# Kernel optimization log

Measured on AMD Instinct MI355X. Metric: run time of the kernel, lower is better.

## Reference

```python
import jax, jax.numpy as jnp
import numpy as np

H = 10  # hidden_size


def _lstm_cell(x, h, c, Wih, Whh, bih, bhh):
    # PyTorch LSTMCell: gates ordered i, f, g, o
    gates = x @ Wih.T + bih + h @ Whh.T + bhh  # [B, 4H]
    i, f, g, o = jnp.split(gates, 4, axis=-1)
    c_new = jax.nn.sigmoid(f) * c + jax.nn.sigmoid(i) * jnp.tanh(g)
    h_new = jax.nn.sigmoid(o) * jnp.tanh(c_new)
    return h_new, c_new


def setup_inputs() -> dict:
    key = jax.random.key(0)
    ks = jax.random.split(key, 12)
    B, T = 16384, 2048
    s = 1.0 / np.sqrt(H)  # PyTorch LSTMCell init scale
    inp = {
        "x": jax.random.normal(ks[0], (B, T, 2), dtype=jnp.float32),
        "WihA": jax.random.uniform(ks[1], (4 * H, 2), minval=-s, maxval=s),
        "WhhA": jax.random.uniform(ks[2], (4 * H, H), minval=-s, maxval=s),
        "bihA": jax.random.uniform(ks[3], (4 * H,), minval=-s, maxval=s),
        "bhhA": jax.random.uniform(ks[4], (4 * H,), minval=-s, maxval=s),
        "WihB": jax.random.uniform(ks[5], (4 * H, 1), minval=-s, maxval=s),
        "WhhB": jax.random.uniform(ks[6], (4 * H, H), minval=-s, maxval=s),
        "bihB": jax.random.uniform(ks[7], (4 * H,), minval=-s, maxval=s),
        "bhhB": jax.random.uniform(ks[8], (4 * H,), minval=-s, maxval=s),
        "Wlin": jax.random.uniform(ks[9], (1, H), minval=-s, maxval=s),
        "blin": jax.random.uniform(ks[10], (1,), minval=-s, maxval=s),
    }
    return inp


def reference(x, WihA, WhhA, bihA, bhhA, WihB, WhhB, bihB, bhhB, Wlin, blin):
    B, T, _ = x.shape
    # time-major pairs: step 2k uses cellB on x[:, 2k, :1], step 2k+1 uses cellA on x[:, 2k+1, :]
    xs = jnp.transpose(x, (1, 0, 2)).reshape(T // 2, 2, B, 2)  # [T/2, 2, B, 2]
    h0 = jnp.zeros((B, H), dtype=x.dtype)
    c0 = jnp.zeros((B, H), dtype=x.dtype)

    def step(carry, x_pair):
        h, c = carry
        h, c = _lstm_cell(x_pair[0][:, :1], h, c, WihB, WhhB, bihB, bhhB)
        h, c = _lstm_cell(x_pair[1], h, c, WihA, WhhA, bihA, bhhA)
        return (h, c), None

    (h, c), _ = jax.lax.scan(step, (h0, c0), xs)
    # original stacks all hx but only uses the last timestep
    return jax.nn.sigmoid(h @ Wlin.T + blin)  # [B, 1]
```

## Files before the change

### kernel.cpp

```cpp
#include <hip/hip_runtime.h>
#include <math.h>

#define H 10
#define BATCH 16384
#define NPAIRS 1024
#define EPW 6

#define LOG2E 1.44269504088896340736f

#if __has_builtin(__builtin_amdgcn_exp2f)
#define EXP2(x) __builtin_amdgcn_exp2f(x)
#else
#define EXP2(x) exp2f(x)
#endif

__device__ __forceinline__ float fast_rcp(float x) { return __builtin_amdgcn_rcpf(x); }

__global__ void __launch_bounds__(64, 2)
lstm_kernel(const float* __restrict__ x,
            const float* __restrict__ WihA, const float* __restrict__ WhhA,
            const float* __restrict__ bihA, const float* __restrict__ bhhA,
            const float* __restrict__ WihB, const float* __restrict__ WhhB,
            const float* __restrict__ bihB, const float* __restrict__ bhhB,
            const float* __restrict__ Wlin, const float* __restrict__ blin,
            float* __restrict__ out)
{
    const int lane    = threadIdx.x;
    const int e_local = lane / H;
    const int j       = lane - e_local * H;
    const bool active = lane < EPW * H;
    const int elem    = blockIdx.x * EPW + e_local;
    const bool valid  = active && (elem < BATCH);
    const int jj      = active ? j : 0;
    const int elem_c  = valid ? elem : 0;

    float wA[4][H], wB[4][H];
    float bA[4], bB[4], wxA0[4], wxA1[4], wxB[4];
#pragma unroll
    for (int g = 0; g < 4; ++g) {
        const float s = (g == 2) ? (2.0f * LOG2E) : (-LOG2E);
        const int row = g * H + jj;
        bA[g]   = s * (bihA[row] + bhhA[row]);
        bB[g]   = s * (bihB[row] + bhhB[row]);
        wxA0[g] = s * WihA[row * 2 + 0];
        wxA1[g] = s * WihA[row * 2 + 1];
        wxB[g]  = s * WihB[row];
#pragma unroll
        for (int k = 0; k < H; ++k) {
            wA[g][k] = s * WhhA[row * H + k];
            wB[g][k] = s * WhhB[row * H + k];
        }
    }
#pragma unroll
    for (int g = 0; g < 4; ++g) {
        asm volatile("" : "+v"(bA[g]), "+v"(bB[g]), "+v"(wxA0[g]),
                          "+v"(wxA1[g]), "+v"(wxB[g]));
#pragma unroll
        for (int k = 0; k < H; ++k) {
            asm volatile("" : "+v"(wA[g][k]), "+v"(wB[g][k]));
        }
    }

    const int base4 = (e_local * H) << 2;
    const float4* __restrict__ xr = (const float4*)x + (size_t)elem_c * NPAIRS;

    float h = 0.0f, c = 0.0f;
    float4 xp = xr[0];

#pragma unroll 2
    for (int p = 0; p < NPAIRS; ++p) {
        const int pn = (p + 1 < NPAIRS) ? (p + 1) : p;
        const float4 xnext = xr[pn];

        {
            float y0 = fmaf(wxB[0], xp.x, bB[0]);
            float y1 = fmaf(wxB[1], xp.x, bB[1]);
            float y2 = fmaf(wxB[2], xp.x, bB[2]);
            float y3 = fmaf(wxB[3], xp.x, bB[3]);
#pragma unroll
            for (int k = 0; k < H; ++k) {
                const float hk = __int_as_float(
                    __builtin_amdgcn_ds_bpermute(base4 + (k << 2), __float_as_int(h)));
                y0 = fmaf(wB[0][k], hk, y0);
                y1 = fmaf(wB[1][k], hk, y1);
                y2 = fmaf(wB[2][k], hk, y2);
                y3 = fmaf(wB[3][k], hk, y3);
            }
            const float ef = EXP2(y1);
            const float ei = EXP2(y0);
            const float eg = EXP2(-__builtin_fabsf(y2));
            const float sf = fast_rcp(1.0f + ef);
            const float d1 = (1.0f + ei) * (1.0f + eg);
            const float it = __builtin_copysignf((1.0f - eg) * fast_rcp(d1), y2);
            const float cn = fmaf(sf, c, it);
            const float eo = EXP2(y3);
            const float ec = EXP2((-2.0f * LOG2E) * __builtin_fabsf(cn));
            const float d2 = (1.0f + eo) * (1.0f + ec);
            h = __builtin_copysignf((1.0f - ec) * fast_rcp(d2), cn);
            c = cn;
        }

        {
            float y0 = fmaf(wxA1[0], xp.w, fmaf(wxA0[0], xp.z, bA[0]));
            float y1 = fmaf(wxA1[1], xp.w, fmaf(wxA0[1], xp.z, bA[1]));
            float y2 = fmaf(wxA1[2], xp.w, fmaf(wxA0[2], xp.z, bA[2]));
            float y3 = fmaf(wxA1[3], xp.w, fmaf(wxA0[3], xp.z, bA[3]));
#pragma unroll
            for (int k = 0; k < H; ++k) {
                const float hk = __int_as_float(
                    __builtin_amdgcn_ds_bpermute(base4 + (k << 2), __float_as_int(h)));
                y0 = fmaf(wA[0][k], hk, y0);
                y1 = fmaf(wA[1][k], hk, y1);
                y2 = fmaf(wA[2][k], hk, y2);
                y3 = fmaf(wA[3][k], hk, y3);
            }
            const float ef = EXP2(y1);
            const float ei = EXP2(y0);
            const float eg = EXP2(-__builtin_fabsf(y2));
            const float sf = fast_rcp(1.0f + ef);
            const float d1 = (1.0f + ei) * (1.0f + eg);
            const float it = __builtin_copysignf((1.0f - eg) * fast_rcp(d1), y2);
            const float cn = fmaf(sf, c, it);
            const float eo = EXP2(y3);
            const float ec = EXP2((-2.0f * LOG2E) * __builtin_fabsf(cn));
            const float d2 = (1.0f + eo) * (1.0f + ec);
            h = __builtin_copysignf((1.0f - ec) * fast_rcp(d2), cn);
            c = cn;
        }

        xp = xnext;
    }

    const float v = Wlin[jj] * h;
    float s = v;
#pragma unroll
    for (int k = 1; k < H; ++k) {
        s += __int_as_float(
            __builtin_amdgcn_ds_bpermute(base4 + (k << 2), __float_as_int(v)));
    }
    if (valid && j == 0) {
        const float y = s + blin[0];
        out[elem] = fast_rcp(1.0f + EXP2(-LOG2E * y));
    }
}

extern "C" void kernel_launch(void* const* d_in, const int* in_sizes, int n_in,
                              void* d_out, int out_size, void* d_ws, size_t ws_size,
                              hipStream_t stream) {
    const float* x    = (const float*)d_in[0];
    const float* WihA = (const float*)d_in[1];
    const float* WhhA = (const float*)d_in[2];
    const float* bihA = (const float*)d_in[3];
    const float* bhhA = (const float*)d_in[4];
    const float* WihB = (const float*)d_in[5];
    const float* WhhB = (const float*)d_in[6];
    const float* bihB = (const float*)d_in[7];
    const float* bhhB = (const float*)d_in[8];
    const float* Wlin = (const float*)d_in[9];
    const float* blin = (const float*)d_in[10];
    float* out = (float*)d_out;

    const int grid = (BATCH + EPW - 1) / EPW;
    hipLaunchKernelGGL(lstm_kernel, dim3(grid), dim3(64), 0, stream,
                       x, WihA, WhhA, bihA, bhhA, WihB, WhhB, bihB, bhhB,
                       Wlin, blin, out);
}
```

Baseline: 1.118 ms.

## Interleave three independent sequence slots per wavefront to hide recurrence latency

Each 64-lane wavefront now carries three batch elements per lane group (16 sequences per wave instead of 6) and steps them together in an interleaved loop. The independent recurrences give the scheduler work to fill the latency of bpermute and the transcendental chain on each serial step. The grid shrinks from about 2731 to 1024 waves. The cost is more registers per lane and fewer waves, which may lower occupancy. The third slot leaves 20 lanes doing redundant work on element 0.

```diff
diff --git a/kernel.cpp b/kernel.cpp
--- a/kernel.cpp
+++ b/kernel.cpp
@@ -4,7 +4,7 @@
 #define H 10
 #define BATCH 16384
 #define NPAIRS 1024
-#define EPW 6
+#define SPW 16
 
 #define LOG2E 1.44269504088896340736f
 
@@ -28,119 +28,149 @@
     const int lane    = threadIdx.x;
     const int e_local = lane / H;
     const int j       = lane - e_local * H;
-    const bool active = lane < EPW * H;
-    const int elem    = blockIdx.x * EPW + e_local;
-    const bool valid  = active && (elem < BATCH);
+    const bool active = lane < 6 * H;
     const int jj      = active ? j : 0;
-    const int elem_c  = valid ? elem : 0;
+    const int g       = active ? e_local : 0;
+
+    const int base  = blockIdx.x * SPW;
+    const int elem0 = base + g;
+    const int elem1 = base + 6 + g;
+    const bool s2   = active && (g < 4);
+    const int elem2 = s2 ? (base + 12 + g) : 0;
 
     float wA[4][H], wB[4][H];
     float bA[4], bB[4], wxA0[4], wxA1[4], wxB[4];
 #pragma unroll
-    for (int g = 0; g < 4; ++g) {
-        const float s = (g == 2) ? (2.0f * LOG2E) : (-LOG2E);
-        const int row = g * H + jj;
-        bA[g]   = s * (bihA[row] + bhhA[row]);
-        bB[g]   = s * (bihB[row] + bhhB[row]);
-        wxA0[g] = s * WihA[row * 2 + 0];
-        wxA1[g] = s * WihA[row * 2 + 1];
-        wxB[g]  = s * WihB[row];
+    for (int q = 0; q < 4; ++q) {
+        const float s = (q == 2) ? (2.0f * LOG2E) : (-LOG2E);
+        const int row = q * H + jj;
+        bA[q]   = s * (bihA[row] + bhhA[row]);
+        bB[q]   = s * (bihB[row] + bhhB[row]);
+        wxA0[q] = s * WihA[row * 2 + 0];
+        wxA1[q] = s * WihA[row * 2 + 1];
+        wxB[q]  = s * WihB[row];
 #pragma unroll
         for (int k = 0; k < H; ++k) {
-            wA[g][k] = s * WhhA[row * H + k];
-            wB[g][k] = s * WhhB[row * H + k];
+            wA[q][k] = s * WhhA[row * H + k];
+            wB[q][k] = s * WhhB[row * H + k];
         }
     }
 #pragma unroll
-    for (int g = 0; g < 4; ++g) {
-        asm volatile("" : "+v"(bA[g]), "+v"(bB[g]), "+v"(wxA0[g]),
-                          "+v"(wxA1[g]), "+v"(wxB[g]));
+    for (int q = 0; q < 4; ++q) {
+        asm volatile("" : "+v"(bA[q]), "+v"(bB[q]), "+v"(wxA0[q]),
+                          "+v"(wxA1[q]), "+v"(wxB[q]));
 #pragma unroll
         for (int k = 0; k < H; ++k) {
-            asm volatile("" : "+v"(wA[g][k]), "+v"(wB[g][k]));
+            asm volatile("" : "+v"(wA[q][k]), "+v"(wB[q][k]));
         }
     }
 
     const int base4 = (e_local * H) << 2;
-    const float4* __restrict__ xr = (const float4*)x + (size_t)elem_c * NPAIRS;
 
-    float h = 0.0f, c = 0.0f;
-    float4 xp = xr[0];
+    const float4* __restrict__ xr0 = (const float4*)x + (size_t)elem0 * NPAIRS;
+    const float4* __restrict__ xr1 = (const float4*)x + (size_t)elem1 * NPAIRS;
+    const float4* __restrict__ xr2 = (const float4*)x + (size_t)elem2 * NPAIRS;
 
-#pragma unroll 2
+    auto cellB = [&](float& h, float& c, float xx) {
+        float y0 = fmaf(wxB[0], xx, bB[0]);
+        float y1 = fmaf(wxB[1], xx, bB[1]);
+        float y2 = fmaf(wxB[2], xx, bB[2]);
+        float y3 = fmaf(wxB[3], xx, bB[3]);
+#pragma unroll
+        for (int k = 0; k < H; ++k) {
+            const float hk = __int_as_float(
+                __builtin_amdgcn_ds_bpermute(base4 + (k << 2), __float_as_int(h)));
+            y0 = fmaf(wB[0][k], hk, y0);
+            y1 = fmaf(wB[1][k], hk, y1);
+            y2 = fmaf(wB[2][k], hk, y2);
+            y3 = fmaf(wB[3][k], hk, y3);
+        }
+        const float ef = EXP2(y1);
+        const float ei = EXP2(y0);
+        const float eg = EXP2(-__builtin_fabsf(y2));
+        const float sf = fast_rcp(1.0f + ef);
+        const float d1 = (1.0f + ei) * (1.0f + eg);
+        const float it = __builtin_copysignf((1.0f - eg) * fast_rcp(d1), y2);
+        const float cn = fmaf(sf, c, it);
+        const float eo = EXP2(y3);
+        const float ec = EXP2((-2.0f * LOG2E) * __builtin_fabsf(cn));
+        const float d2 = (1.0f + eo) * (1.0f + ec);
+        h = __builtin_copysignf((1.0f - ec) * fast_rcp(d2), cn);
+        c = cn;
+    };
+
+    auto cellA = [&](float& h, float& c, float x0, float x1) {
+        float y0 = fmaf(wxA1[0], x1, fmaf(wxA0[0], x0, bA[0]));
+        float y1 = fmaf(wxA1[1], x1, fmaf(wxA0[1], x0, bA[1]));
+        float y2 = fmaf(wxA1[2], x1, fmaf(wxA0[2], x0, bA[2]));
+        float y3 = fmaf(wxA1[3], x1, fmaf(wxA0[3], x0, bA[3]));
+#pragma unroll
+        for (int k = 0; k < H; ++k) {
+            const float hk = __int_as_float(
+                __builtin_amdgcn_ds_bpermute(base4 + (k << 2), __float_as_int(h)));
+            y0 = fmaf(wA[0][k], hk, y0);
+            y1 = fmaf(wA[1][k], hk, y1);
+            y2 = fmaf(wA[2][k], hk, y2);
+            y3 = fmaf(wA[3][k], hk, y3);
+        }
+        const float ef = EXP2(y1);
+        const float ei = EXP2(y0);
+        const float eg = EXP2(-__builtin_fabsf(y2));
+        const float sf = fast_rcp(1.0f + ef);
+        const float d1 = (1.0f + ei) * (1.0f + eg);
+        const float it = __builtin_copysignf((1.0f - eg) * fast_rcp(d1), y2);
+        const float cn = fmaf(sf, c, it);
+        const float eo = EXP2(y3);
+        const float ec = EXP2((-2.0f * LOG2E) * __builtin_fabsf(cn));
+        const float d2 = (1.0f + eo) * (1.0f + ec);
+        h = __builtin_copysignf((1.0f - ec) * fast_rcp(d2), cn);
+        c = cn;
+    };
+
+    float h0 = 0.0f, c0 = 0.0f;
+    float h1 = 0.0f, c1 = 0.0f;
+    float h2 = 0.0f, c2 = 0.0f;
+    float4 xp0 = xr0[0], xp1 = xr1[0], xp2 = xr2[0];
+
+#pragma unroll 1
     for (int p = 0; p < NPAIRS; ++p) {
         const int pn = (p + 1 < NPAIRS) ? (p + 1) : p;
-        const float4 xnext = xr[pn];
+        const float4 xn0 = xr0[pn];
+        const float4 xn1 = xr1[pn];
+        const float4 xn2 = xr2[pn];
 
-        {
-            float y0 = fmaf(wxB[0], xp.x, bB[0]);
-            float y1 = fmaf(wxB[1], xp.x, bB[1]);
-            float y2 = fmaf(wxB[2], xp.x, bB[2]);
-            float y3 = fmaf(wxB[3], xp.x, bB[3]);
-#pragma unroll
-            for (int k = 0; k < H; ++k) {
-                const float hk = __int_as_float(
-                    __builtin_amdgcn_ds_bpermute(base4 + (k << 2), __float_as_int(h)));
-                y0 = fmaf(wB[0][k], hk, y0);
-                y1 = fmaf(wB[1][k], hk, y1);
-                y2 = fmaf(wB[2][k], hk, y2);
-                y3 = fmaf(wB[3][k], hk, y3);
-            }
-            const float ef = EXP2(y1);
-            const float ei = EXP2(y0);
-            const float eg = EXP2(-__builtin_fabsf(y2));
-            const float sf = fast_rcp(1.0f + ef);
-            const float d1 = (1.0f + ei) * (1.0f + eg);
-            const float it = __builtin_copysignf((1.0f - eg) * fast_rcp(d1), y2);
-            const float cn = fmaf(sf, c, it);
-            const float eo = EXP2(y3);
-            const float ec = EXP2((-2.0f * LOG2E) * __builtin_fabsf(cn));
-            const float d2 = (1.0f + eo) * (1.0f + ec);
-            h = __builtin_copysignf((1.0f - ec) * fast_rcp(d2), cn);
-            c = cn;
-        }
+        cellB(h0, c0, xp0.x);
+        cellB(h1, c1, xp1.x);
+        cellB(h2, c2, xp2.x);
 
-        {
-            float y0 = fmaf(wxA1[0], xp.w, fmaf(wxA0[0], xp.z, bA[0]));
-            float y1 = fmaf(wxA1[1], xp.w, fmaf(wxA0[1], xp.z, bA[1]));
-            float y2 = fmaf(wxA1[2], xp.w, fmaf(wxA0[2], xp.z, bA[2]));
-            float y3 = fmaf(wxA1[3], xp.w, fmaf(wxA0[3], xp.z, bA[3]));
-#pragma unroll
-            for (int k = 0; k < H; ++k) {
-                const float hk = __int_as_float(
-                    __builtin_amdgcn_ds_bpermute(base4 + (k << 2), __float_as_int(h)));
-                y0 = fmaf(wA[0][k], hk, y0);
-                y1 = fmaf(wA[1][k], hk, y1);
-                y2 = fmaf(wA[2][k], hk, y2);
-                y3 = fmaf(wA[3][k], hk, y3);
-            }
-            const float ef = EXP2(y1);
-            const float ei = EXP2(y0);
-            const float eg = EXP2(-__builtin_fabsf(y2));
-            const float sf = fast_rcp(1.0f + ef);
-            const float d1 = (1.0f + ei) * (1.0f + eg);
-            const float it = __builtin_copysignf((1.0f - eg) * fast_rcp(d1), y2);
-            const float cn = fmaf(sf, c, it);
-            const float eo = EXP2(y3);
-            const float ec = EXP2((-2.0f * LOG2E) * __builtin_fabsf(cn));
-            const float d2 = (1.0f + eo) * (1.0f + ec);
-            h = __builtin_copysignf((1.0f - ec) * fast_rcp(d2), cn);
-            c = cn;
-        }
+        cellA(h0, c0, xp0.z, xp0.w);
+        cellA(h1, c1, xp1.z, xp1.w);
+        cellA(h2, c2, xp2.z, xp2.w);
 
-        xp = xnext;
+        xp0 = xn0; xp1 = xn1; xp2 = xn2;
     }
 
-    const float v = Wlin[jj] * h;
-    float s = v;
+    auto reduce10 = [&](float hv) -> float {
+        const float v = Wlin[jj] * hv;
+        float s = v;
 #pragma unroll
-    for (int k = 1; k < H; ++k) {
-        s += __int_as_float(
-            __builtin_amdgcn_ds_bpermute(base4 + (k << 2), __float_as_int(v)));
-    }
-    if (valid && j == 0) {
-        const float y = s + blin[0];
-        out[elem] = fast_rcp(1.0f + EXP2(-LOG2E * y));
+        for (int k = 1; k < H; ++k) {
+            s += __int_as_float(
+                __builtin_amdgcn_ds_bpermute(base4 + (k << 2), __float_as_int(v)));
+        }
+        return s;
+    };
+
+    const float s0 = reduce10(h0);
+    const float s1 = reduce10(h1);
+    const float s2v = reduce10(h2);
+
+    if (active && j == 0) {
+        const float bl = blin[0];
+        out[elem0] = fast_rcp(1.0f + EXP2(-LOG2E * (s0 + bl)));
+        out[elem1] = fast_rcp(1.0f + EXP2(-LOG2E * (s1 + bl)));
+        if (g < 4)
+            out[elem2] = fast_rcp(1.0f + EXP2(-LOG2E * (s2v + bl)));
     }
 }
 
@@ -160,7 +190,7 @@
     const float* blin = (const float*)d_in[10];
     float* out = (float*)d_out;
 
-    const int grid = (BATCH + EPW - 1) / EPW;
+    const int grid = BATCH / SPW;
     hipLaunchKernelGGL(lstm_kernel, dim3(grid), dim3(64), 0, stream,
                        x, WihA, WhhA, bihA, bhhA, WihB, WhhB, bihB, bhhB,
                        Wlin, blin, out);
```

Result: slower. 3.048 ms (+172.7%).
